# Kernel optimization log

Measured on AMD Instinct MI355X. Metric: run time of the kernel, lower is better.

Reference implementation:

```python
import jax, jax.numpy as jnp
import numpy as np

N_LAYERS = 2
N_QUBITS = 8
N_MEASURE = 5
DIM = 2 ** N_QUBITS  # 256


def _ry(state, half_theta, wire):
    # Apply RY(theta) = [[cos(t/2), -sin(t/2)], [sin(t/2), cos(t/2)]] on `wire`.
    # Statevector is real (all gates real, initial state real).
    B = state.shape[0]
    st = state.reshape(B, 2 ** wire, 2, 2 ** (N_QUBITS - wire - 1))
    c = jnp.cos(half_theta)[:, None, None]
    s = jnp.sin(half_theta)[:, None, None]
    a0, a1 = st[:, :, 0], st[:, :, 1]
    st = jnp.stack([c * a0 - s * a1, s * a0 + c * a1], axis=2)
    return st.reshape(B, DIM)


def _cnot(state, ctrl):
    # CNOT on wires [ctrl, ctrl+1]: flip target amplitudes where control=1.
    B = state.shape[0]
    st = state.reshape(B, 2 ** ctrl, 2, 2, 2 ** (N_QUBITS - ctrl - 2))
    st = jnp.stack([st[:, :, 0], st[:, :, 1, ::-1]], axis=2)
    return st.reshape(B, DIM)


def setup_inputs() -> dict:
    key = jax.random.key(0)
    k1, k2, k3 = jax.random.split(key, 3)
    B, F = 131072, 16
    inputs = jax.random.normal(k1, (B, F), dtype=jnp.float32)
    weights = jax.random.normal(k2, (N_LAYERS, N_QUBITS), dtype=jnp.float32)
    scalings = jax.random.normal(k3, (N_LAYERS, N_QUBITS), dtype=jnp.float32)
    return {"inputs": inputs, "weights": weights, "scalings": scalings}


def reference(inputs, weights, scalings):
    B, F = inputs.shape
    # |0...0> initial state
    state = jnp.zeros((B, DIM), dtype=inputs.dtype).at[:, 0].set(1.0)
    for layer in range(N_LAYERS):
        start = (layer * N_QUBITS) % F
        for i in range(N_QUBITS):
            fi = (start + i) % F
            theta = weights[layer, i] + scalings[layer, i] * inputs[:, fi]
            state = _ry(state, 0.5 * theta, i)
        for i in range(N_QUBITS - 1):
            state = _cnot(state, i)
    # probs over wires 0..N_MEASURE-1 (marginalize trailing wires)
    probs = (state * state).reshape(B, 2 ** N_MEASURE, 2 ** (N_QUBITS - N_MEASURE)).sum(-1)
    return probs
```

## Files before the change

### kernel.cpp

```cpp
#include <hip/hip_runtime.h>


constexpr int F = 16;

struct Sym { float P, Q, R; };
struct Ent { float up, uq, ur, vp, vq, vr, t, tr2; };
struct Eff { float A, B, C, D, E, Fc, G, H; };

__device__ __forceinline__ Ent mk_ent(float c1, float s1, float c2, float s2) {
    const float u = c2 * c2, v = s2 * s2, t = c2 * s2;
    const float p = c1 * c1, q = s1 * s1, r = c1 * s1;
    Ent e;
    e.up = u * p; e.uq = u * q; e.ur = u * r;
    e.vp = v * p; e.vq = v * q; e.vr = v * r;
    e.t  = t;     e.tr2 = 2.0f * t * r;
    return e;
}

template <int Z>
__device__ __forceinline__ Sym apply_z(const Ent& e, const Sym& s) {
    if (Z == 0) {
        return Sym{ fmaf(e.up, s.P, fmaf(-e.tr2, s.Q, e.vq * s.R)),
                    fmaf(e.ur, s.P, fmaf(-e.t,   s.Q, e.vr * s.R)),
                    fmaf(e.uq, s.P, fmaf(-e.tr2, s.Q, e.vp * s.R)) };
    } else {
        return Sym{ fmaf(e.vp, s.P, fmaf( e.tr2, s.Q, e.uq * s.R)),
                    fmaf(e.vr, s.P, fmaf( e.t,   s.Q, e.ur * s.R)),
                    fmaf(e.vq, s.P, fmaf( e.tr2, s.Q, e.up * s.R)) };
    }
}

__device__ __forceinline__ Eff mk_eff(const Ent& e, bool z) {
    Eff f;
    f.A = z ? e.vp  :  e.up;   f.B = z ? e.tr2 : -e.tr2;
    f.C = z ? e.uq  :  e.vq;   f.D = z ? e.vr  :  e.ur;
    f.E = z ? e.t   : -e.t;    f.Fc= z ? e.ur  :  e.vr;
    f.G = z ? e.vq  :  e.uq;   f.H = z ? e.up  :  e.vp;
    return f;
}
__device__ __forceinline__ Eff flip_eff(const Eff& e) {
    return Eff{ e.H, -e.B, e.G, e.Fc, -e.E, e.D, e.C, e.A };
}
__device__ __forceinline__ Sym apply_eff(const Eff& e, const Sym& s) {
    return Sym{ fmaf(e.A, s.P, fmaf(e.B, s.Q, e.C  * s.R)),
                fmaf(e.D, s.P, fmaf(e.E, s.Q, e.Fc * s.R)),
                fmaf(e.G, s.P, fmaf(e.B, s.Q, e.H  * s.R)) };
}

__global__ __launch_bounds__(256) void qnn_mps4_kernel(
    const float* __restrict__ inputs,
    const float* __restrict__ weights,
    const float* __restrict__ scalings,
    float* __restrict__ out, int B)
{
    const int g = blockIdx.x * 256 + threadIdx.x;
    const int b = g >> 2;
    const int t = g & 3;
    if (b >= B) return;

    const bool z0 = (t >> 1) & 1;
    const bool z1 = ((t ^ (t >> 1)) & 1);
    const bool tb = (t & 1);

    const float4* in4 = reinterpret_cast<const float4*>(inputs) + (size_t)b * 4;
    const float4 xa = in4[0], xb = in4[1], xc = in4[2], xd = in4[3];
    const float x[16] = { xa.x, xa.y, xa.z, xa.w,  xb.x, xb.y, xb.z, xb.w,
                          xc.x, xc.y, xc.z, xc.w,  xd.x, xd.y, xd.z, xd.w };

    float c1[5], s1[5], c2[5], s2[5];
    #pragma unroll
    for (int w = 0; w < 5; ++w) {
        const float t1 = weights[w]     + scalings[w]     * x[w];
        const float t2 = weights[8 + w] + scalings[8 + w] * x[8 + w];
        __sincosf(0.5f * t1, &s1[w], &c1[w]);
        __sincosf(0.5f * t2, &s2[w], &c2[w]);
    }
    const float th5 = weights[5] + scalings[5] * x[5];
    const float s5  = __sinf(th5);

    const Sym r5{ 1.0f, s5, 1.0f };

    const Ent e4 = mk_ent(c1[4], s1[4], c2[4], s2[4]);
    Sym r4[2];
    r4[0] = apply_z<0>(e4, r5);
    r4[1] = apply_z<1>(e4, r5);

    const Ent e3 = mk_ent(c1[3], s1[3], c2[3], s2[3]);
    Sym r3[4];
    r3[0] = apply_z<0>(e3, r4[0]);  r3[1] = apply_z<0>(e3, r4[1]);
    r3[2] = apply_z<1>(e3, r4[0]);  r3[3] = apply_z<1>(e3, r4[1]);

    const Ent e2 = mk_ent(c1[2], s1[2], c2[2], s2[2]);
    const Eff e2a = mk_eff(e2, tb);
    const Eff e2b = flip_eff(e2a);
    Sym r2p[8];
    #pragma unroll
    for (int j = 0; j < 4; ++j) {
        r2p[j]     = apply_eff(e2a, r3[j]);
        r2p[4 + j] = apply_eff(e2b, r3[j]);
    }

    const Eff e1e = mk_eff(mk_ent(c1[1], s1[1], c2[1], s2[1]), z1);
    const Ent e0  = mk_ent(c1[0], s1[0], c2[0], s2[0]);
    const float A0 = z0 ? e0.vp  :  e0.up;
    const float B0 = z0 ? e0.tr2 : -e0.tr2;
    const float C0 = z0 ? e0.uq  :  e0.vq;

    float pr[8];
    #pragma unroll
    for (int u = 0; u < 8; ++u) {
        constexpr int gray[8] = {0, 1, 3, 2, 6, 7, 5, 4};
        const Sym v = apply_eff(e1e, r2p[gray[u]]);
        pr[u] = fmaf(A0, v.P, fmaf(B0, v.Q, C0 * v.R));
    }

    float4* o4 = reinterpret_cast<float4*>(out) + (size_t)b * 8 + (size_t)t * 2;
    o4[0] = make_float4(pr[0], pr[1], pr[2], pr[3]);
    o4[1] = make_float4(pr[4], pr[5], pr[6], pr[7]);
}

extern "C" void kernel_launch(void* const* d_in, const int* in_sizes, int n_in,
                              void* d_out, int out_size, void* d_ws, size_t ws_size,
                              hipStream_t stream) {
    const float* inputs   = (const float*)d_in[0];
    const float* weights  = (const float*)d_in[1];
    const float* scalings = (const float*)d_in[2];
    float* out = (float*)d_out;
    const int B = in_sizes[0] / F;
    const int total = B * 4;
    const int grid = (total + 255) / 256;
    qnn_mps4_kernel<<<grid, 256, 0, stream>>>(inputs, weights, scalings, out, B);
}
```

Before: 68.57 us.

## Contract left environment first and dot with right tensors per output

Restructures the contraction so the left-side factors from wires 0-2 are multiplied into two small left vectors, then each output is a 3-term dot product with the right-side r3 tensors. This replaces eight applications of the wire-1 and wire-0 transfer steps on intermediate tensors. It also drops the unused fourth float4 load in favour of a single scalar load and adds a min-blocks hint to launch bounds. The kernel is likely memory-bound, so the arithmetic savings may matter little.

```diff
diff --git a/kernel.cpp b/kernel.cpp
--- a/kernel.cpp
+++ b/kernel.cpp
@@ -41,13 +41,13 @@
 __device__ __forceinline__ Eff flip_eff(const Eff& e) {
     return Eff{ e.H, -e.B, e.G, e.Fc, -e.E, e.D, e.C, e.A };
 }
-__device__ __forceinline__ Sym apply_eff(const Eff& e, const Sym& s) {
-    return Sym{ fmaf(e.A, s.P, fmaf(e.B, s.Q, e.C  * s.R)),
-                fmaf(e.D, s.P, fmaf(e.E, s.Q, e.Fc * s.R)),
-                fmaf(e.G, s.P, fmaf(e.B, s.Q, e.H  * s.R)) };
+__device__ __forceinline__ Sym lmul(const Sym& l, const Eff& e) {
+    return Sym{ fmaf(e.A, l.P, fmaf(e.D, l.Q, e.G * l.R)),
+                fmaf(e.B, l.P + l.R, e.E * l.Q),
+                fmaf(e.C, l.P, fmaf(e.Fc, l.Q, e.H * l.R)) };
 }
 
-__global__ __launch_bounds__(256) void qnn_mps4_kernel(
+__global__ __launch_bounds__(256, 8) void qnn_lr_kernel(
     const float* __restrict__ inputs,
     const float* __restrict__ weights,
     const float* __restrict__ scalings,
@@ -63,23 +63,24 @@
     const bool tb = (t & 1);
 
     const float4* in4 = reinterpret_cast<const float4*>(inputs) + (size_t)b * 4;
-    const float4 xa = in4[0], xb = in4[1], xc = in4[2], xd = in4[3];
-    const float x[16] = { xa.x, xa.y, xa.z, xa.w,  xb.x, xb.y, xb.z, xb.w,
-                          xc.x, xc.y, xc.z, xc.w,  xd.x, xd.y, xd.z, xd.w };
+    const float4 xa = in4[0], xb = in4[1], xc = in4[2];
+    const float x12 = inputs[(size_t)b * F + 12];
+
+    const float xs1[5] = { xa.x, xa.y, xa.z, xa.w, xb.x };
+    const float xs2[5] = { xc.x, xc.y, xc.z, xc.w, x12 };
 
     float c1[5], s1[5], c2[5], s2[5];
     #pragma unroll
     for (int w = 0; w < 5; ++w) {
-        const float t1 = weights[w]     + scalings[w]     * x[w];
-        const float t2 = weights[8 + w] + scalings[8 + w] * x[8 + w];
+        const float t1 = weights[w]     + scalings[w]     * xs1[w];
+        const float t2 = weights[8 + w] + scalings[8 + w] * xs2[w];
         __sincosf(0.5f * t1, &s1[w], &c1[w]);
         __sincosf(0.5f * t2, &s2[w], &c2[w]);
     }
-    const float th5 = weights[5] + scalings[5] * x[5];
+    const float th5 = weights[5] + scalings[5] * xb.y;
     const float s5  = __sinf(th5);
 
     const Sym r5{ 1.0f, s5, 1.0f };
-
     const Ent e4 = mk_ent(c1[4], s1[4], c2[4], s2[4]);
     Sym r4[2];
     r4[0] = apply_z<0>(e4, r5);
@@ -90,28 +91,26 @@
     r3[0] = apply_z<0>(e3, r4[0]);  r3[1] = apply_z<0>(e3, r4[1]);
     r3[2] = apply_z<1>(e3, r4[0]);  r3[3] = apply_z<1>(e3, r4[1]);
 
-    const Ent e2 = mk_ent(c1[2], s1[2], c2[2], s2[2]);
-    const Eff e2a = mk_eff(e2, tb);
+    const Ent e0 = mk_ent(c1[0], s1[0], c2[0], s2[0]);
+    const Sym l0{ z0 ? e0.vp  :  e0.up,
+                  z0 ? e0.tr2 : -e0.tr2,
+                  z0 ? e0.uq  :  e0.vq };
+    const Eff e1e = mk_eff(mk_ent(c1[1], s1[1], c2[1], s2[1]), z1);
+    const Sym l1 = lmul(l0, e1e);
+    const Eff e2a = mk_eff(mk_ent(c1[2], s1[2], c2[2], s2[2]), tb);
     const Eff e2b = flip_eff(e2a);
-    Sym r2p[8];
-    #pragma unroll
-    for (int j = 0; j < 4; ++j) {
-        r2p[j]     = apply_eff(e2a, r3[j]);
-        r2p[4 + j] = apply_eff(e2b, r3[j]);
-    }
-
-    const Eff e1e = mk_eff(mk_ent(c1[1], s1[1], c2[1], s2[1]), z1);
-    const Ent e0  = mk_ent(c1[0], s1[0], c2[0], s2[0]);
-    const float A0 = z0 ? e0.vp  :  e0.up;
-    const float B0 = z0 ? e0.tr2 : -e0.tr2;
-    const float C0 = z0 ? e0.uq  :  e0.vq;
+    const Sym lA = lmul(l1, e2a);
+    const Sym lB = lmul(l1, e2b);
 
     float pr[8];
     #pragma unroll
     for (int u = 0; u < 8; ++u) {
-        constexpr int gray[8] = {0, 1, 3, 2, 6, 7, 5, 4};
-        const Sym v = apply_eff(e1e, r2p[gray[u]]);
-        pr[u] = fmaf(A0, v.P, fmaf(B0, v.Q, C0 * v.R));
+        const int u2 = (u >> 2) & 1;
+        const int z3 = ((u >> 1) ^ (u >> 2)) & 1;
+        const int z4 = (u ^ (u >> 1)) & 1;
+        const Sym& l = u2 ? lB : lA;
+        const Sym& r = r3[(z3 << 1) | z4];
+        pr[u] = fmaf(l.P, r.P, fmaf(l.Q, r.Q, l.R * r.R));
     }
 
     float4* o4 = reinterpret_cast<float4*>(out) + (size_t)b * 8 + (size_t)t * 2;
@@ -129,5 +128,5 @@
     const int B = in_sizes[0] / F;
     const int total = B * 4;
     const int grid = (total + 255) / 256;
-    qnn_mps4_kernel<<<grid, 256, 0, stream>>>(inputs, weights, scalings, out, B);
+    qnn_lr_kernel<<<grid, 256, 0, stream>>>(inputs, weights, scalings, out, B);
 }
```

Result: no change. 68.15 us (-0.6%).
